# Optimization experiments

Hardware: AMD Instinct MI355X
Metric: run time of the kernel (lower is better)

Reference implementation:

```python
import jax, jax.numpy as jnp
import numpy as np

DEFAULT_MASK_VALUE = -0.7 * float(np.finfo(np.float32).max)

B, S, HQ, HKV, D = 2, 2048, 16, 8, 128
CHUNK = 512


def _chunk_causal_mask(seq_len, chunk_size):
    # True where attention allowed: same chunk AND causal within chunk.
    row = jax.lax.broadcasted_iota(jnp.int32, (seq_len, seq_len), 0)
    col = jax.lax.broadcasted_iota(jnp.int32, (seq_len, seq_len), 1)
    return (row // chunk_size == col // chunk_size) & (row >= col)


def _block_mask_indices(bidirectional_mask):
    # [B, L] 0/1 -> segment ids, e.g. [0,1,1,1,0,0,1,1,0,1,0] -> [0,1,1,1,0,0,2,2,0,3,0]
    m = bidirectional_mask.astype(jnp.int32)
    padded = jnp.pad(m, [(0, 0), (1, 0)], constant_values=0)
    boundary = padded[..., 1:] > padded[..., :-1]
    return m * jnp.cumsum(boundary, axis=-1)


def _bidirectional_block_mask(bidirectional_mask):
    idx = _block_mask_indices(bidirectional_mask)  # [B, L]
    return (idx[:, None, :] == idx[:, :, None]) & (idx[:, :, None] > 0)  # [B, L, L]


def setup_inputs() -> dict:
    key = jax.random.key(0)
    kq, kk, kv, kb = jax.random.split(key, 4)
    q = jax.random.normal(kq, (B, S, HQ, D), dtype=jnp.float32)
    k = jax.random.normal(kk, (B, S, HKV, D), dtype=jnp.float32)
    v = jax.random.normal(kv, (B, S, HKV, D), dtype=jnp.float32)
    bidirectional_mask = jax.random.randint(kb, (B, S), 0, 2, dtype=jnp.int32)
    return {"q": q, "k": k, "v": v, "bidirectional_mask": bidirectional_mask,
            "chunk_size": CHUNK}


def reference(q, k, v, bidirectional_mask, chunk_size):
    b, s, hq, d = q.shape
    hkv = k.shape[2]
    group = hq // hkv  # GQA group size
    scale = 1.0 / jnp.sqrt(jnp.asarray(d, q.dtype))

    # [b, s, hkv, group, d]
    qg = q.reshape(b, s, hkv, group, d) * scale
    # logits: [b, hkv, group, q, kv]
    logits = jnp.einsum("bqhgd,bkhd->bhgqk", qg, k)

    # combined mask: chunked-causal OR bidirectional block (image tokens attend
    # bidirectionally within their contiguous block)
    chunk_mask = _chunk_causal_mask(s, chunk_size)                 # [s, s]
    bidir_mask = _bidirectional_block_mask(bidirectional_mask)    # [b, s, s]
    allowed = chunk_mask[None, :, :] | bidir_mask                  # [b, s, s]
    allowed = allowed[:, None, None, :, :]                         # [b, 1, 1, s, s]

    masked = jnp.where(allowed, logits, DEFAULT_MASK_VALUE)
    probs = jax.nn.softmax(masked, axis=-1)

    out = jnp.einsum("bhgqk,bkhd->bqhgd", probs, v)
    return out.reshape(b, s, hq, d)
```

## Files before the change

kernel.cpp:

```cpp
#include <hip/hip_runtime.h>
#include <hip/hip_bf16.h>

#define SLEN 2048
#define BATCH 2
#define NHQ 16
#define NHKV 8
#define DIM 128
#define SEG 512
#define NSEG (SLEN / SEG)
#define KVROW (NHKV * DIM)

#define KSTR 68
#define VSTR 36
#define PSTR 72

typedef __attribute__((ext_vector_type(8))) short bf16x8;
typedef __attribute__((ext_vector_type(4))) float f32x4;

static __device__ inline short f2bf(float f) {
    __hip_bfloat16 h = __float2bfloat16(f);
    return *reinterpret_cast<short*>(&h);
}
static __device__ inline unsigned pack_bf2(float lo, float hi) {
    unsigned a = (unsigned)(unsigned short)f2bf(lo);
    unsigned b = (unsigned)(unsigned short)f2bf(hi);
    return a | (b << 16);
}
static __device__ inline float fast_exp2(float x) {
#if __has_builtin(__builtin_amdgcn_exp2f)
    return __builtin_amdgcn_exp2f(x);
#else
    return __builtin_exp2f(x);
#endif
}

__global__ void prep_runs(const int* __restrict__ mask,
                          int* __restrict__ rs, int* __restrict__ re) {
    __shared__ int sm[SLEN];
    const int b = blockIdx.x;
    const int* mb = mask + b * SLEN;
    for (int i = threadIdx.x; i < SLEN; i += blockDim.x) sm[i] = mb[i];
    __syncthreads();
    for (int i = threadIdx.x; i < SLEN; i += blockDim.x) {
        int s0 = -1, e0 = -2;
        if (sm[i] == 1) {
            s0 = i; while (s0 > 0 && sm[s0 - 1] == 1) --s0;
            e0 = i; while (e0 < SLEN - 1 && sm[e0 + 1] == 1) ++e0;
        }
        rs[b * SLEN + i] = s0;
        re[b * SLEN + i] = e0;
    }
}

__global__ __launch_bounds__(256, 2) void attn_fwd(
    const float* __restrict__ Q, const float* __restrict__ K,
    const float* __restrict__ V, const int* __restrict__ rs,
    const int* __restrict__ re, const int* __restrict__ csp,
    float* __restrict__ Out)
{
    const int tid  = threadIdx.x;
    const int wid  = tid >> 6;
    const int lane = tid & 63;
    const int quad = lane >> 4;
    const int n    = lane & 15;

    const int bid = blockIdx.x;
    const int xcd = bid & 7;
    const int M   = (bid >> 3) & 7;
    const int Ghi = bid >> 6;
    const int G   = Ghi * 8 + xcd;
    const int seg = G & 3;
    const int h   = (G >> 2) & 7;
    const int b   = G >> 5;
    const int par2 = M >> 1;
    const int hq  = h * 2 + (M & 1);

    const int rbase = seg * SEG;
    int r0[2];
    r0[0] = rbase + (4 * wid + par2) * 16;
    r0[1] = r0[0] + 256;

    __shared__ unsigned kt[2][64 * KSTR];
    __shared__ unsigned vt[2][128 * VSTR];
    __shared__ short    pls[4][16 * PSTR];
    __shared__ int      smk[2][64];
    __shared__ int      wred[8];

    const float scale = 0.08838834764831845f * 1.4426950408889634f;
    const int cs = csp[0];

    const int* rsb = rs + b * SLEN;
    const int* reb = re + b * SLEN;

    int lo_rt[2], hi_rt[2], rsrv[2][4], csg[2][4], cshi[2];
    #pragma unroll
    for (int u = 0; u < 2; ++u) {
        const int row = r0[u] + n;
        const int rsv = rsb[row];
        const int rev = reb[row];
        const int csr = (row / cs) * cs;
        int lo = csr; if (rsv >= 0 && rsv < lo) lo = rsv;
        int hi = row; if (rev > hi) hi = rev;
        #pragma unroll
        for (int off = 8; off > 0; off >>= 1) {
            lo = min(lo, __shfl_xor(lo, off, 64));
            hi = max(hi, __shfl_xor(hi, off, 64));
        }
        lo_rt[u] = lo; hi_rt[u] = hi;
        #pragma unroll
        for (int g = 0; g < 4; ++g) {
            const int r = r0[u] + quad * 4 + g;
            rsrv[u][g] = rsb[r];
            csg[u][g]  = (r / cs) * cs;
        }
        cshi[u] = ((r0[u] + 15) / cs) * cs;
    }

    bf16x8 qa[2][4];
    #pragma unroll
    for (int u = 0; u < 2; ++u) {
        const float* qp = Q + (((size_t)(b * SLEN + r0[u] + n) * NHQ + hq) * DIM) + quad * 8;
        #pragma unroll
        for (int kb = 0; kb < 4; ++kb) {
            float4 f0 = *(const float4*)(qp + kb * 32);
            float4 f1 = *(const float4*)(qp + kb * 32 + 4);
            bf16x8 a;
            a[0] = f2bf(f0.x * scale); a[1] = f2bf(f0.y * scale);
            a[2] = f2bf(f0.z * scale); a[3] = f2bf(f0.w * scale);
            a[4] = f2bf(f1.x * scale); a[5] = f2bf(f1.y * scale);
            a[6] = f2bf(f1.z * scale); a[7] = f2bf(f1.w * scale);
            qa[u][kb] = a;
        }
    }

    if (lane == 0) {
        wred[wid * 2]     = min(lo_rt[0], lo_rt[1]);
        wred[wid * 2 + 1] = max(hi_rt[0], hi_rt[1]);
    }
    __syncthreads();
    int lo_blk = 0x7fffffff, hi_blk = 0;
    #pragma unroll
    for (int i = 0; i < 4; ++i) {
        lo_blk = min(lo_blk, wred[2 * i]);
        hi_blk = max(hi_blk, wred[2 * i + 1]);
    }
    lo_blk &= ~63;

    float lrow[2][4];
    f32x4 o[2][8];
    #pragma unroll
    for (int u = 0; u < 2; ++u) {
        #pragma unroll
        for (int g = 0; g < 4; ++g) lrow[u][g] = 0.0f;
        #pragma unroll
        for (int nb = 0; nb < 8; ++nb) o[u][nb] = (f32x4){0.f, 0.f, 0.f, 0.f};
    }

    const float* Kb = K + ((size_t)b * SLEN * NHKV + h) * DIM;
    const float* Vb = V + ((size_t)b * SLEN * NHKV + h) * DIM;

    const int krow8 = tid >> 3;
    const int kcol  = (tid & 7) * 16;
    const int vd    = tid & 127;
    const int vkey0 = (tid >> 7) * 32;

    float4 kr[8];
    float  vr[32];
    int    rsn = 0;

    {
        const float* kpa = Kb + (size_t)min(lo_blk + krow8, SLEN - 1) * KVROW + kcol;
        const float* kpb = Kb + (size_t)min(lo_blk + krow8 + 32, SLEN - 1) * KVROW + kcol;
        kr[0] = ((const float4*)kpa)[0]; kr[1] = ((const float4*)kpa)[1];
        kr[2] = ((const float4*)kpa)[2]; kr[3] = ((const float4*)kpa)[3];
        kr[4] = ((const float4*)kpb)[0]; kr[5] = ((const float4*)kpb)[1];
        kr[6] = ((const float4*)kpb)[2]; kr[7] = ((const float4*)kpb)[3];
        #pragma unroll
        for (int i = 0; i < 32; ++i)
            vr[i] = Vb[(size_t)min(lo_blk + vkey0 + i, SLEN - 1) * KVROW + vd];
        if (tid < 64) rsn = rsb[min(lo_blk + tid, SLEN - 1)];
    }

    int bufi = 0;
    for (int k0 = lo_blk; k0 <= hi_blk; k0 += 64, bufi ^= 1) {
        {
            uint4* kda = (uint4*)&kt[bufi][krow8 * KSTR + (tid & 7) * 8];
            kda[0] = make_uint4(pack_bf2(kr[0].x, kr[0].y), pack_bf2(kr[0].z, kr[0].w),
                                pack_bf2(kr[1].x, kr[1].y), pack_bf2(kr[1].z, kr[1].w));
            kda[1] = make_uint4(pack_bf2(kr[2].x, kr[2].y), pack_bf2(kr[2].z, kr[2].w),
                                pack_bf2(kr[3].x, kr[3].y), pack_bf2(kr[3].z, kr[3].w));
            uint4* kdb = (uint4*)&kt[bufi][(krow8 + 32) * KSTR + (tid & 7) * 8];
            kdb[0] = make_uint4(pack_bf2(kr[4].x, kr[4].y), pack_bf2(kr[4].z, kr[4].w),
                                pack_bf2(kr[5].x, kr[5].y), pack_bf2(kr[5].z, kr[5].w));
            kdb[1] = make_uint4(pack_bf2(kr[6].x, kr[6].y), pack_bf2(kr[6].z, kr[6].w),
                                pack_bf2(kr[7].x, kr[7].y), pack_bf2(kr[7].z, kr[7].w));
            uint4* vw = (uint4*)&vt[bufi][vd * VSTR + (tid >> 7) * 16];
            #pragma unroll
            for (int j = 0; j < 4; ++j)
                vw[j] = make_uint4(pack_bf2(vr[8 * j + 0], vr[8 * j + 1]),
                                   pack_bf2(vr[8 * j + 2], vr[8 * j + 3]),
                                   pack_bf2(vr[8 * j + 4], vr[8 * j + 5]),
                                   pack_bf2(vr[8 * j + 6], vr[8 * j + 7]));
            if (tid < 64) smk[bufi][tid] = rsn;
        }
        __syncthreads();

        if (k0 + 64 <= hi_blk) {
            const int kn0 = k0 + 64;
            const float* kpa = Kb + (size_t)min(kn0 + krow8, SLEN - 1) * KVROW + kcol;
            const float* kpb = Kb + (size_t)min(kn0 + krow8 + 32, SLEN - 1) * KVROW + kcol;
            kr[0] = ((const float4*)kpa)[0]; kr[1] = ((const float4*)kpa)[1];
            kr[2] = ((const float4*)kpa)[2]; kr[3] = ((const float4*)kpa)[3];
            kr[4] = ((const float4*)kpb)[0]; kr[5] = ((const float4*)kpb)[1];
            kr[6] = ((const float4*)kpb)[2]; kr[7] = ((const float4*)kpb)[3];
            #pragma unroll
            for (int i = 0; i < 32; ++i)
                vr[i] = Vb[(size_t)min(kn0 + vkey0 + i, SLEN - 1) * KVROW + vd];
            if (tid < 64) rsn = rsb[min(kn0 + tid, SLEN - 1)];
        }

        bool act[2];
        act[0] = (k0 + 63 >= lo_rt[0]) && (k0 <= hi_rt[0]);
        act[1] = (k0 + 63 >= lo_rt[1]) && (k0 <= hi_rt[1]);
        if (!act[0] && !act[1]) continue;

        const short* ktb = (const short*)&kt[bufi][0];
        const short* vtb = (const short*)&vt[bufi][0];

        f32x4 sfr[2][4];
        #pragma unroll
        for (int u = 0; u < 2; ++u)
            #pragma unroll
            for (int c = 0; c < 4; ++c)
                sfr[u][c] = (f32x4){0.f, 0.f, 0.f, 0.f};
        #pragma unroll
        for (int c = 0; c < 4; ++c) {
            #pragma unroll
            for (int kb = 0; kb < 4; ++kb) {
                bf16x8 kf = *(const bf16x8*)(ktb + (c * 16 + n) * 136 + kb * 32 + quad * 8);
                if (act[0]) sfr[0][c] = __builtin_amdgcn_mfma_f32_16x16x32_bf16(qa[0][kb], kf, sfr[0][c], 0, 0, 0);
                if (act[1]) sfr[1][c] = __builtin_amdgcn_mfma_f32_16x16x32_bf16(qa[1][kb], kf, sfr[1][c], 0, 0, 0);
            }
        }

        int rskv[4];
        #pragma unroll
        for (int c = 0; c < 4; ++c) rskv[c] = smk[bufi][c * 16 + n];

        #pragma unroll
        for (int u = 0; u < 2; ++u) {
            if (!act[u]) continue;
            const bool fullc = (k0 >= cshi[u]) && (k0 + 63 <= r0[u]);
            if (!fullc) {
                #pragma unroll
                for (int c = 0; c < 4; ++c) {
                    const int kcl = k0 + c * 16 + n;
                    #pragma unroll
                    for (int g = 0; g < 4; ++g) {
                        const int r = r0[u] + quad * 4 + g;
                        const bool ok = ((kcl >= csg[u][g]) && (kcl <= r)) ||
                                        (rsrv[u][g] >= 0 && rskv[c] == rsrv[u][g]);
                        if (!ok) sfr[u][c][g] = -3.0e38f;
                    }
                }
            }
            float psum[4] = {0.f, 0.f, 0.f, 0.f};
            #pragma unroll
            for (int c = 0; c < 4; ++c) {
                #pragma unroll
                for (int g = 0; g < 4; ++g) {
                    const float pv = fast_exp2(sfr[u][c][g]);
                    psum[g] += pv;
                    pls[wid][(quad * 4 + g) * PSTR + c * 16 + n] = f2bf(pv);
                }
            }
            #pragma unroll
            for (int g = 0; g < 4; ++g) lrow[u][g] += psum[g];

            #pragma unroll
            for (int kb2 = 0; kb2 < 2; ++kb2) {
                bf16x8 pa = *(const bf16x8*)&pls[wid][n * PSTR + kb2 * 32 + quad * 8];
                #pragma unroll
                for (int nb = 0; nb < 8; ++nb) {
                    bf16x8 vf = *(const bf16x8*)(vtb + (nb * 16 + n) * 72 + kb2 * 32 + quad * 8);
                    o[u][nb] = __builtin_amdgcn_mfma_f32_16x16x32_bf16(pa, vf, o[u][nb], 0, 0, 0);
                }
            }
        }
    }

    #pragma unroll
    for (int u = 0; u < 2; ++u) {
        #pragma unroll
        for (int g = 0; g < 4; ++g) {
            float l = lrow[u][g];
            #pragma unroll
            for (int off = 8; off > 0; off >>= 1)
                l += __shfl_xor(l, off, 64);
            const float inv = 1.0f / l;
            const int r = r0[u] + quad * 4 + g;
            float* op = Out + ((size_t)(b * SLEN + r) * NHQ + hq) * DIM + n;
            #pragma unroll
            for (int nb = 0; nb < 8; ++nb)
                op[nb * 16] = o[u][nb][g] * inv;
        }
    }
}

extern "C" void kernel_launch(void* const* d_in, const int* in_sizes, int n_in,
                              void* d_out, int out_size, void* d_ws, size_t ws_size,
                              hipStream_t stream) {
    const float* q  = (const float*)d_in[0];
    const float* k  = (const float*)d_in[1];
    const float* v  = (const float*)d_in[2];
    const int*   bm = (const int*)d_in[3];
    const int*   cs = (const int*)d_in[4];
    float* out = (float*)d_out;

    int* rs = (int*)d_ws;
    int* re = rs + BATCH * SLEN;

    hipLaunchKernelGGL(prep_runs, dim3(BATCH), dim3(256), 0, stream, bm, rs, re);
    hipLaunchKernelGGL(attn_fwd, dim3(BATCH * NHQ * NSEG * 4), dim3(256), 0, stream,
                       q, k, v, rs, re, cs, out);
}
```

Measured before the change: 153.7 us.

## Use 512-thread blocks with one row tile per wave and XOR-swizzled LDS

Each block now runs 8 waves of 512 threads. Every wave owns a single 16-row query tile instead of two, so per-thread registers for Q, the accumulators and the staged K/V loads are halved. The padded shared-memory strides are replaced by XOR-swizzled layouts to avoid bank conflicts. Per-key mask ids are now distributed through shuffles rather than a shared array, and s_setprio is raised around the MFMA sections. The risk is that each wave now does less work to hide its latency, and the bounds clamps on K/V loads were removed.

```diff
diff --git a/kernel.cpp b/kernel.cpp
--- a/kernel.cpp
+++ b/kernel.cpp
@@ -10,9 +10,9 @@
 #define NSEG (SLEN / SEG)
 #define KVROW (NHKV * DIM)
 
-#define KSTR 68
-#define VSTR 36
-#define PSTR 72
+#define KTD (64 * 64)
+#define VTD (128 * 32)
+#define PLSD (16 * 32)
 
 typedef __attribute__((ext_vector_type(8))) short bf16x8;
 typedef __attribute__((ext_vector_type(4))) float f32x4;
@@ -52,7 +52,7 @@
     }
 }
 
-__global__ __launch_bounds__(256, 2) void attn_fwd(
+__global__ __launch_bounds__(512, 4) void attn_fwd(
     const float* __restrict__ Q, const float* __restrict__ K,
     const float* __restrict__ V, const int* __restrict__ rs,
     const int* __restrict__ re, const int* __restrict__ csp,
@@ -67,24 +67,20 @@
     const int bid = blockIdx.x;
     const int xcd = bid & 7;
     const int M   = (bid >> 3) & 7;
-    const int Ghi = bid >> 6;
-    const int G   = Ghi * 8 + xcd;
+    const int G   = (bid >> 6) * 8 + xcd;
     const int seg = G & 3;
     const int h   = (G >> 2) & 7;
     const int b   = G >> 5;
-    const int par2 = M >> 1;
+    const int par = M >> 1;
     const int hq  = h * 2 + (M & 1);
 
     const int rbase = seg * SEG;
-    int r0[2];
-    r0[0] = rbase + (4 * wid + par2) * 16;
-    r0[1] = r0[0] + 256;
-
-    __shared__ unsigned kt[2][64 * KSTR];
-    __shared__ unsigned vt[2][128 * VSTR];
-    __shared__ short    pls[4][16 * PSTR];
-    __shared__ int      smk[2][64];
-    __shared__ int      wred[8];
+    const int r0 = rbase + (4 * wid + par) * 16;
+
+    __shared__ unsigned pool[2 * KTD + 2 * VTD + 8 * PLSD];
+    unsigned* ktp = pool;
+    unsigned* vtp = pool + 2 * KTD;
+    short*    pw  = (short*)(pool + 2 * KTD + 2 * VTD) + wid * (16 * 64);
 
     const float scale = 0.08838834764831845f * 1.4426950408889634f;
     const int cs = csp[0];
@@ -92,34 +88,26 @@
     const int* rsb = rs + b * SLEN;
     const int* reb = re + b * SLEN;
 
-    int lo_rt[2], hi_rt[2], rsrv[2][4], csg[2][4], cshi[2];
-    #pragma unroll
-    for (int u = 0; u < 2; ++u) {
-        const int row = r0[u] + n;
-        const int rsv = rsb[row];
-        const int rev = reb[row];
-        const int csr = (row / cs) * cs;
-        int lo = csr; if (rsv >= 0 && rsv < lo) lo = rsv;
-        int hi = row; if (rev > hi) hi = rev;
+    const int row  = r0 + n;
+    const int rsvq = rsb[row];
+    const int csrq = (row / cs) * cs;
+    int lo_rt, hi_rt;
+    {
+        const int revq = reb[row];
+        int lo = csrq; if (rsvq >= 0 && rsvq < lo) lo = rsvq;
+        int hi = row;  if (revq > hi) hi = revq;
         #pragma unroll
         for (int off = 8; off > 0; off >>= 1) {
             lo = min(lo, __shfl_xor(lo, off, 64));
             hi = max(hi, __shfl_xor(hi, off, 64));
         }
-        lo_rt[u] = lo; hi_rt[u] = hi;
-        #pragma unroll
-        for (int g = 0; g < 4; ++g) {
-            const int r = r0[u] + quad * 4 + g;
-            rsrv[u][g] = rsb[r];
-            csg[u][g]  = (r / cs) * cs;
-        }
-        cshi[u] = ((r0[u] + 15) / cs) * cs;
-    }
-
-    bf16x8 qa[2][4];
-    #pragma unroll
-    for (int u = 0; u < 2; ++u) {
-        const float* qp = Q + (((size_t)(b * SLEN + r0[u] + n) * NHQ + hq) * DIM) + quad * 8;
+        lo_rt = lo; hi_rt = hi;
+    }
+    const int cshi = ((r0 + 15) / cs) * cs;
+
+    bf16x8 qa[4];
+    {
+        const float* qp = Q + (((size_t)(b * SLEN + row) * NHQ + hq) * DIM) + quad * 8;
         #pragma unroll
         for (int kb = 0; kb < 4; ++kb) {
             float4 f0 = *(const float4*)(qp + kb * 32);
@@ -129,181 +117,176 @@
             a[2] = f2bf(f0.z * scale); a[3] = f2bf(f0.w * scale);
             a[4] = f2bf(f1.x * scale); a[5] = f2bf(f1.y * scale);
             a[6] = f2bf(f1.z * scale); a[7] = f2bf(f1.w * scale);
-            qa[u][kb] = a;
-        }
-    }
-
-    if (lane == 0) {
-        wred[wid * 2]     = min(lo_rt[0], lo_rt[1]);
-        wred[wid * 2 + 1] = max(hi_rt[0], hi_rt[1]);
-    }
-    __syncthreads();
-    int lo_blk = 0x7fffffff, hi_blk = 0;
+            qa[kb] = a;
+        }
+    }
+
+    int lo_blk, hi_blk;
+    {
+        int* sred = (int*)pool;
+        if (lane == 0) { sred[wid * 2] = lo_rt; sred[wid * 2 + 1] = hi_rt; }
+        __syncthreads();
+        int lo = 0x7fffffff, hi = 0;
+        #pragma unroll
+        for (int i = 0; i < 8; ++i) {
+            lo = min(lo, sred[2 * i]);
+            hi = max(hi, sred[2 * i + 1]);
+        }
+        __syncthreads();
+        lo_blk = lo & ~63;
+        hi_blk = hi;
+    }
+
+    float lrow[4] = {0.f, 0.f, 0.f, 0.f};
+    f32x4 o[8];
     #pragma unroll
-    for (int i = 0; i < 4; ++i) {
-        lo_blk = min(lo_blk, wred[2 * i]);
-        hi_blk = max(hi_blk, wred[2 * i + 1]);
-    }
-    lo_blk &= ~63;
-
-    float lrow[2][4];
-    f32x4 o[2][8];
-    #pragma unroll
-    for (int u = 0; u < 2; ++u) {
-        #pragma unroll
-        for (int g = 0; g < 4; ++g) lrow[u][g] = 0.0f;
-        #pragma unroll
-        for (int nb = 0; nb < 8; ++nb) o[u][nb] = (f32x4){0.f, 0.f, 0.f, 0.f};
-    }
+    for (int nb = 0; nb < 8; ++nb) o[nb] = (f32x4){0.f, 0.f, 0.f, 0.f};
 
     const float* Kb = K + ((size_t)b * SLEN * NHKV + h) * DIM;
     const float* Vb = V + ((size_t)b * SLEN * NHKV + h) * DIM;
 
-    const int krow8 = tid >> 3;
-    const int kcol  = (tid & 7) * 16;
-    const int vd    = tid & 127;
-    const int vkey0 = (tid >> 7) * 32;
-
-    float4 kr[8];
-    float  vr[32];
-    int    rsn = 0;
+    const int krow = tid >> 3;
+    const int kc8  = tid & 7;
+    const int vd   = tid & 127;
+    const int vg   = tid >> 7;
+
+    float4 kr[4];
+    float  vr[16];
+    int    rsv_c;
 
     {
-        const float* kpa = Kb + (size_t)min(lo_blk + krow8, SLEN - 1) * KVROW + kcol;
-        const float* kpb = Kb + (size_t)min(lo_blk + krow8 + 32, SLEN - 1) * KVROW + kcol;
-        kr[0] = ((const float4*)kpa)[0]; kr[1] = ((const float4*)kpa)[1];
-        kr[2] = ((const float4*)kpa)[2]; kr[3] = ((const float4*)kpa)[3];
-        kr[4] = ((const float4*)kpb)[0]; kr[5] = ((const float4*)kpb)[1];
-        kr[6] = ((const float4*)kpb)[2]; kr[7] = ((const float4*)kpb)[3];
-        #pragma unroll
-        for (int i = 0; i < 32; ++i)
-            vr[i] = Vb[(size_t)min(lo_blk + vkey0 + i, SLEN - 1) * KVROW + vd];
-        if (tid < 64) rsn = rsb[min(lo_blk + tid, SLEN - 1)];
-    }
+        const float* kp = Kb + (size_t)(lo_blk + krow) * KVROW + kc8 * 16;
+        kr[0] = ((const float4*)kp)[0]; kr[1] = ((const float4*)kp)[1];
+        kr[2] = ((const float4*)kp)[2]; kr[3] = ((const float4*)kp)[3];
+        const float* vp = Vb + (size_t)(lo_blk + vg * 16) * KVROW + vd;
+        #pragma unroll
+        for (int i = 0; i < 16; ++i) vr[i] = vp[(size_t)i * KVROW];
+        rsv_c = rsb[lo_blk + lane];
+    }
+
+    const unsigned kx  = (unsigned)((krow & 7) << 2);
+    const unsigned vx  = (unsigned)((vd & 7) << 2);
+    const unsigned kxr = (unsigned)((n & 7) << 2);
 
     int bufi = 0;
     for (int k0 = lo_blk; k0 <= hi_blk; k0 += 64, bufi ^= 1) {
         {
-            uint4* kda = (uint4*)&kt[bufi][krow8 * KSTR + (tid & 7) * 8];
-            kda[0] = make_uint4(pack_bf2(kr[0].x, kr[0].y), pack_bf2(kr[0].z, kr[0].w),
-                                pack_bf2(kr[1].x, kr[1].y), pack_bf2(kr[1].z, kr[1].w));
-            kda[1] = make_uint4(pack_bf2(kr[2].x, kr[2].y), pack_bf2(kr[2].z, kr[2].w),
-                                pack_bf2(kr[3].x, kr[3].y), pack_bf2(kr[3].z, kr[3].w));
-            uint4* kdb = (uint4*)&kt[bufi][(krow8 + 32) * KSTR + (tid & 7) * 8];
-            kdb[0] = make_uint4(pack_bf2(kr[4].x, kr[4].y), pack_bf2(kr[4].z, kr[4].w),
-                                pack_bf2(kr[5].x, kr[5].y), pack_bf2(kr[5].z, kr[5].w));
-            kdb[1] = make_uint4(pack_bf2(kr[6].x, kr[6].y), pack_bf2(kr[6].z, kr[6].w),
-                                pack_bf2(kr[7].x, kr[7].y), pack_bf2(kr[7].z, kr[7].w));
-            uint4* vw = (uint4*)&vt[bufi][vd * VSTR + (tid >> 7) * 16];
-            #pragma unroll
-            for (int j = 0; j < 4; ++j)
-                vw[j] = make_uint4(pack_bf2(vr[8 * j + 0], vr[8 * j + 1]),
-                                   pack_bf2(vr[8 * j + 2], vr[8 * j + 3]),
-                                   pack_bf2(vr[8 * j + 4], vr[8 * j + 5]),
-                                   pack_bf2(vr[8 * j + 6], vr[8 * j + 7]));
-            if (tid < 64) smk[bufi][tid] = rsn;
+            unsigned* kd = ktp + bufi * KTD;
+            const unsigned kb0 = (unsigned)(krow * 64 + kc8 * 8);
+            *(uint4*)(kd + ((kb0)     ^ kx)) =
+                make_uint4(pack_bf2(kr[0].x, kr[0].y), pack_bf2(kr[0].z, kr[0].w),
+                           pack_bf2(kr[1].x, kr[1].y), pack_bf2(kr[1].z, kr[1].w));
+            *(uint4*)(kd + ((kb0 + 4) ^ kx)) =
+                make_uint4(pack_bf2(kr[2].x, kr[2].y), pack_bf2(kr[2].z, kr[2].w),
+                           pack_bf2(kr[3].x, kr[3].y), pack_bf2(kr[3].z, kr[3].w));
+            unsigned* vdp = vtp + bufi * VTD;
+            const unsigned vb0 = (unsigned)(vd * 32 + vg * 8);
+            *(uint4*)(vdp + ((vb0)     ^ vx)) =
+                make_uint4(pack_bf2(vr[0], vr[1]),  pack_bf2(vr[2], vr[3]),
+                           pack_bf2(vr[4], vr[5]),  pack_bf2(vr[6], vr[7]));
+            *(uint4*)(vdp + ((vb0 + 4) ^ vx)) =
+                make_uint4(pack_bf2(vr[8], vr[9]),  pack_bf2(vr[10], vr[11]),
+                           pack_bf2(vr[12], vr[13]), pack_bf2(vr[14], vr[15]));
         }
         __syncthreads();
 
+        int rsv_n = rsv_c;
         if (k0 + 64 <= hi_blk) {
             const int kn0 = k0 + 64;
-            const float* kpa = Kb + (size_t)min(kn0 + krow8, SLEN - 1) * KVROW + kcol;
-            const float* kpb = Kb + (size_t)min(kn0 + krow8 + 32, SLEN - 1) * KVROW + kcol;
-            kr[0] = ((const float4*)kpa)[0]; kr[1] = ((const float4*)kpa)[1];
-            kr[2] = ((const float4*)kpa)[2]; kr[3] = ((const float4*)kpa)[3];
-            kr[4] = ((const float4*)kpb)[0]; kr[5] = ((const float4*)kpb)[1];
-            kr[6] = ((const float4*)kpb)[2]; kr[7] = ((const float4*)kpb)[3];
-            #pragma unroll
-            for (int i = 0; i < 32; ++i)
-                vr[i] = Vb[(size_t)min(kn0 + vkey0 + i, SLEN - 1) * KVROW + vd];
-            if (tid < 64) rsn = rsb[min(kn0 + tid, SLEN - 1)];
-        }
-
-        bool act[2];
-        act[0] = (k0 + 63 >= lo_rt[0]) && (k0 <= hi_rt[0]);
-        act[1] = (k0 + 63 >= lo_rt[1]) && (k0 <= hi_rt[1]);
-        if (!act[0] && !act[1]) continue;
-
-        const short* ktb = (const short*)&kt[bufi][0];
-        const short* vtb = (const short*)&vt[bufi][0];
-
-        f32x4 sfr[2][4];
-        #pragma unroll
-        for (int u = 0; u < 2; ++u)
-            #pragma unroll
-            for (int c = 0; c < 4; ++c)
-                sfr[u][c] = (f32x4){0.f, 0.f, 0.f, 0.f};
-        #pragma unroll
-        for (int c = 0; c < 4; ++c) {
-            #pragma unroll
-            for (int kb = 0; kb < 4; ++kb) {
-                bf16x8 kf = *(const bf16x8*)(ktb + (c * 16 + n) * 136 + kb * 32 + quad * 8);
-                if (act[0]) sfr[0][c] = __builtin_amdgcn_mfma_f32_16x16x32_bf16(qa[0][kb], kf, sfr[0][c], 0, 0, 0);
-                if (act[1]) sfr[1][c] = __builtin_amdgcn_mfma_f32_16x16x32_bf16(qa[1][kb], kf, sfr[1][c], 0, 0, 0);
+            const float* kp = Kb + (size_t)(kn0 + krow) * KVROW + kc8 * 16;
+            kr[0] = ((const float4*)kp)[0]; kr[1] = ((const float4*)kp)[1];
+            kr[2] = ((const float4*)kp)[2]; kr[3] = ((const float4*)kp)[3];
+            const float* vp = Vb + (size_t)(kn0 + vg * 16) * KVROW + vd;
+            #pragma unroll
+            for (int i = 0; i < 16; ++i) vr[i] = vp[(size_t)i * KVROW];
+            rsv_n = rsb[kn0 + lane];
+        }
+
+        if ((k0 + 63 >= lo_rt) && (k0 <= hi_rt)) {
+            const unsigned* ktb = ktp + bufi * KTD;
+            const unsigned* vtb = vtp + bufi * VTD;
+
+            f32x4 sfr[4];
+            #pragma unroll
+            for (int c = 0; c < 4; ++c) sfr[c] = (f32x4){0.f, 0.f, 0.f, 0.f};
+            __builtin_amdgcn_s_setprio(1);
+            #pragma unroll
+            for (int c = 0; c < 4; ++c) {
+                #pragma unroll
+                for (int kb = 0; kb < 4; ++kb) {
+                    const bf16x8 kf = *(const bf16x8*)(ktb +
+                        (((unsigned)((c * 16 + n) * 64 + kb * 16 + quad * 4)) ^ kxr));
+                    sfr[c] = __builtin_amdgcn_mfma_f32_16x16x32_bf16(qa[kb], kf, sfr[c], 0, 0, 0);
+                }
             }
-        }
-
-        int rskv[4];
-        #pragma unroll
-        for (int c = 0; c < 4; ++c) rskv[c] = smk[bufi][c * 16 + n];
-
-        #pragma unroll
-        for (int u = 0; u < 2; ++u) {
-            if (!act[u]) continue;
-            const bool fullc = (k0 >= cshi[u]) && (k0 + 63 <= r0[u]);
+            __builtin_amdgcn_s_setprio(0);
+
+            const bool fullc = (k0 >= cshi) && (k0 + 63 <= r0);
             if (!fullc) {
+                int rsr[4], csr_g[4];
+                #pragma unroll
+                for (int g = 0; g < 4; ++g) {
+                    rsr[g]   = __shfl(rsvq, quad * 4 + g, 64);
+                    csr_g[g] = __shfl(csrq, quad * 4 + g, 64);
+                }
                 #pragma unroll
                 for (int c = 0; c < 4; ++c) {
-                    const int kcl = k0 + c * 16 + n;
+                    const int kcl  = k0 + c * 16 + n;
+                    const int rskv = __shfl(rsv_c, c * 16 + n, 64);
                     #pragma unroll
                     for (int g = 0; g < 4; ++g) {
-                        const int r = r0[u] + quad * 4 + g;
-                        const bool ok = ((kcl >= csg[u][g]) && (kcl <= r)) ||
-                                        (rsrv[u][g] >= 0 && rskv[c] == rsrv[u][g]);
-                        if (!ok) sfr[u][c][g] = -3.0e38f;
+                        const int r = r0 + quad * 4 + g;
+                        const bool ok = ((kcl >= csr_g[g]) && (kcl <= r)) ||
+                                        (rsr[g] >= 0 && rskv == rsr[g]);
+                        if (!ok) sfr[c][g] = -3.0e38f;
                     }
                 }
             }
+
             float psum[4] = {0.f, 0.f, 0.f, 0.f};
             #pragma unroll
             for (int c = 0; c < 4; ++c) {
                 #pragma unroll
                 for (int g = 0; g < 4; ++g) {
-                    const float pv = fast_exp2(sfr[u][c][g]);
+                    const float pv = fast_exp2(sfr[c][g]);
                     psum[g] += pv;
-                    pls[wid][(quad * 4 + g) * PSTR + c * 16 + n] = f2bf(pv);
+                    const int prow = quad * 4 + g;
+                    pw[((unsigned)(prow * 64 + c * 16 + n)) ^ ((unsigned)((prow & 7) << 3))] = f2bf(pv);
                 }
             }
             #pragma unroll
-            for (int g = 0; g < 4; ++g) lrow[u][g] += psum[g];
-
+            for (int g = 0; g < 4; ++g) lrow[g] += psum[g];
+
+            __builtin_amdgcn_s_setprio(1);
             #pragma unroll
             for (int kb2 = 0; kb2 < 2; ++kb2) {
-                bf16x8 pa = *(const bf16x8*)&pls[wid][n * PSTR + kb2 * 32 + quad * 8];
+                const bf16x8 pa = *(const bf16x8*)(pw +
+                    (((unsigned)(n * 64 + kb2 * 32 + quad * 8)) ^ ((unsigned)((n & 7) << 3))));
                 #pragma unroll
                 for (int nb = 0; nb < 8; ++nb) {
-                    bf16x8 vf = *(const bf16x8*)(vtb + (nb * 16 + n) * 72 + kb2 * 32 + quad * 8);
-                    o[u][nb] = __builtin_amdgcn_mfma_f32_16x16x32_bf16(pa, vf, o[u][nb], 0, 0, 0);
+                    const bf16x8 vf = *(const bf16x8*)(vtb +
+                        (((unsigned)((nb * 16 + n) * 32 + kb2 * 16 + quad * 4)) ^ kxr));
+                    o[nb] = __builtin_amdgcn_mfma_f32_16x16x32_bf16(pa, vf, o[nb], 0, 0, 0);
                 }
             }
-        }
+            __builtin_amdgcn_s_setprio(0);
+        }
+
+        rsv_c = rsv_n;
     }
 
     #pragma unroll
-    for (int u = 0; u < 2; ++u) {
-        #pragma unroll
-        for (int g = 0; g < 4; ++g) {
-            float l = lrow[u][g];
-            #pragma unroll
-            for (int off = 8; off > 0; off >>= 1)
-                l += __shfl_xor(l, off, 64);
-            const float inv = 1.0f / l;
-            const int r = r0[u] + quad * 4 + g;
-            float* op = Out + ((size_t)(b * SLEN + r) * NHQ + hq) * DIM + n;
-            #pragma unroll
-            for (int nb = 0; nb < 8; ++nb)
-                op[nb * 16] = o[u][nb][g] * inv;
-        }
+    for (int g = 0; g < 4; ++g) {
+        float l = lrow[g];
+        #pragma unroll
+        for (int off = 8; off > 0; off >>= 1)
+            l += __shfl_xor(l, off, 64);
+        const float inv = 1.0f / l;
+        const int r = r0 + quad * 4 + g;
+        float* op = Out + ((size_t)(b * SLEN + r) * NHQ + hq) * DIM + n;
+        #pragma unroll
+        for (int nb = 0; nb < 8; ++nb)
+            op[nb * 16] = o[nb][g] * inv;
     }
 }
 
@@ -321,6 +304,6 @@
     int* re = rs + BATCH * SLEN;
 
     hipLaunchKernelGGL(prep_runs, dim3(BATCH), dim3(256), 0, stream, bm, rs, re);
-    hipLaunchKernelGGL(attn_fwd, dim3(BATCH * NHQ * NSEG * 4), dim3(256), 0, stream,
+    hipLaunchKernelGGL(attn_fwd, dim3(BATCH * NHQ * NSEG * 4), dim3(512), 0, stream,
                        q, k, v, rs, re, cs, out);
 }
```

Measured after the change: 287.2 us. 86.9% more time.
